# Optimization experiments

Measured on AMD Instinct MI355X. Metric: run time of the kernel, lower is better.

The kernel has to match this reference:

```python
import jax, jax.numpy as jnp
import numpy as np

H = 4096          # hidden_size
I = 11008         # intermediate_size
G = 128           # AWQ group_size
# AWQ interleaved nibble order within each packed int32
_ORDER = jnp.array([0, 4, 1, 5, 2, 6, 3, 7], dtype=jnp.int32) * 4


def _mk_lin(key, K, N):
    k1, k2, k3 = jax.random.split(key, 3)
    qw = jax.random.randint(k1, (K, N // 8), 0, 100, dtype=jnp.int32)
    qz = jax.random.randint(k2, (K // G, N // 8), 0, 100, dtype=jnp.int32)
    sc = jax.random.normal(k3, (K // G, N), dtype=jnp.float32) * 0.02
    return qw, qz, sc


def setup_inputs() -> dict:
    key = jax.random.key(0)
    ks = jax.random.split(key, 7)
    x = jax.random.normal(ks[0], (8, 16, H), dtype=jnp.float32)
    ln1_w = jnp.ones((H,), dtype=jnp.float32)
    ln2_w = jnp.ones((H,), dtype=jnp.float32)
    qkv_qw, qkv_qz, qkv_sc = _mk_lin(ks[1], H, 3 * H)
    o_qw, o_qz, o_sc = _mk_lin(ks[2], H, H)
    gu_qw, gu_qz, gu_sc = _mk_lin(ks[3], H, 2 * I)
    dn_qw, dn_qz, dn_sc = _mk_lin(ks[4], I, H)
    return dict(x=x, ln1_w=ln1_w, ln2_w=ln2_w,
                qkv_qw=qkv_qw, qkv_qz=qkv_qz, qkv_sc=qkv_sc,
                o_qw=o_qw, o_qz=o_qz, o_sc=o_sc,
                gu_qw=gu_qw, gu_qz=gu_qz, gu_sc=gu_sc,
                dn_qw=dn_qw, dn_qz=dn_qz, dn_sc=dn_sc)


def rmsnorm(x, w, eps=1e-6):
    return x * jax.lax.rsqrt(jnp.mean(x * x, axis=-1, keepdims=True) + eps) * w


def dequant(qw, qz, sc):
    # qw: [K, N//8] int32 -> [K, N]; qz: [K//G, N//8] -> [K//G, N]
    K = qw.shape[0]
    N = sc.shape[1]
    w = ((qw[:, :, None] >> _ORDER) & 0xF).reshape(K, N).astype(sc.dtype)
    z = ((qz[:, :, None] >> _ORDER) & 0xF).reshape(K // G, N).astype(sc.dtype)
    return (w - jnp.repeat(z, G, axis=0)) * jnp.repeat(sc, G, axis=0)


def lite_linear(x, qw, qz, sc):
    return x @ dequant(qw, qz, sc)


def reference(x, ln1_w, ln2_w,
              qkv_qw, qkv_qz, qkv_sc,
              o_qw, o_qz, o_sc,
              gu_qw, gu_qz, gu_sc,
              dn_qw, dn_qz, dn_sc):
    residual = x
    h = rmsnorm(x, ln1_w)
    h = lite_linear(h, qkv_qw, qkv_qz, qkv_sc)[..., :H]  # mock attn: take q slice
    h = lite_linear(h, o_qw, o_qz, o_sc)
    h = residual + h
    residual = h
    h = rmsnorm(h, ln2_w)
    gate_up = lite_linear(h, gu_qw, gu_qz, gu_sc)
    gate, up = gate_up[..., :I], gate_up[..., I:]
    h = lite_linear(jax.nn.silu(gate) * up, dn_qw, dn_qz, dn_sc)
    return residual + h
```

## Files before the change

kernel.cpp:

```cpp
#include <hip/hip_runtime.h>

typedef unsigned int   u32;
typedef unsigned short u16;

typedef _Float16 h2  __attribute__((ext_vector_type(2)));
typedef _Float16 h8  __attribute__((ext_vector_type(8)));
typedef float    f32x4 __attribute__((ext_vector_type(4)));

#define M_TOK 128

__device__ __forceinline__ u16 f2h_(float f) {
    _Float16 h = (_Float16)f; return __builtin_bit_cast(u16, h);
}
__device__ __forceinline__ float h2f_(u16 b) {
    _Float16 h = __builtin_bit_cast(_Float16, b); return (float)h;
}
__device__ __forceinline__ void acc8(uint4 v, float* s) {
#pragma unroll
    for (int i = 0; i < 4; ++i) {
        u32 w = ((const u32*)&v)[i];
        s[2 * i]     += h2f_((u16)(w & 0xFFFF));
        s[2 * i + 1] += h2f_((u16)(w >> 16));
    }
}

__constant__ int SHC[8] = {0, 16, 4, 20, 8, 24, 12, 28};

__launch_bounds__(256)
__global__ void pack_zs(const int* __restrict__ qz, const float* __restrict__ sc,
                        u32* __restrict__ zs, int qws, int scs, int Ncols, int total) {
    const int idx = blockIdx.x * 256 + threadIdx.x;
    if (idx >= total) return;
    const int g = idx / Ncols, n = idx - g * Ncols;
    const u32 d = (u32)qz[(size_t)g * qws + (n >> 3)];
    const u32 zj = (d >> SHC[n & 7]) & 15u;
    const u32 mz = 0xE400u | zj;
    const u16 sh = f2h_(sc[(size_t)g * scs + n]);
    zs[(size_t)g * Ncols + n] = mz | ((u32)sh << 16);
}


__launch_bounds__(256)
__global__ void rmsnorm_k(const float* __restrict__ in, const float* __restrict__ w,
                          u16* __restrict__ out) {
    const int row = blockIdx.x;
    const float* x = in + (size_t)row * 4096;
    float ss = 0.f;
#pragma unroll
    for (int j = 0; j < 16; ++j) {
        float v = x[threadIdx.x + 256 * j];
        ss += v * v;
    }
#pragma unroll
    for (int off = 32; off > 0; off >>= 1) ss += __shfl_down(ss, off, 64);
    __shared__ float ws4[4];
    if ((threadIdx.x & 63) == 0) ws4[threadIdx.x >> 6] = ss;
    __syncthreads();
    float total = ws4[0] + ws4[1] + ws4[2] + ws4[3];
    float r = rsqrtf(total * (1.f / 4096.f) + 1e-6f);
    const int mt = row >> 4, l16 = row & 15;
#pragma unroll
    for (int c2 = 0; c2 < 2; ++c2) {
        int c = threadIdx.x * 2 + c2;
        int kb = c >> 2, qq = c & 3;
        u16 o8[8];
#pragma unroll
        for (int j = 0; j < 8; ++j) {
            int i = c * 8 + j;
            o8[j] = f2h_(x[i] * r * w[i]);
        }
        *(uint4*)(out + ((size_t)(kb * 8 + mt) * 64 + qq * 16 + l16) * 8) = *(const uint4*)o8;
    }
}

__launch_bounds__(256, 2)
__global__ void gemm_awq(const u16* __restrict__ A, const u32* __restrict__ zs,
                         const int* __restrict__ qw, u16* __restrict__ part,
                         int qws, int N, int K, int kchunk) {
    __shared__ __align__(16) char ldsB[4 * 4608];

    const int tid = threadIdx.x, w = tid >> 6, lane = tid & 63;
    const int q = lane >> 4, l16 = lane & 15;
    const int n0w = blockIdx.x * 128 + w * 32;
    const int pc0 = n0w >> 3;
    const int kp = lane & 31, h = lane >> 5;
    const int sk = blockIdx.y, kc0 = sk * kchunk, kend = min(kc0 + kchunk, K);

    char* myB   = ldsB + w * 4608;
    char* wbase = myB + kp * 4;
    const u16* Ala = A + lane * 8;
    const int* qws_base = qw + pc0;
    const u32* zsA = zs + n0w + h * 8;
    const u32* zsB = zs + n0w + 16 + h * 8;

    f32x4 acc[8][2] = {};
    uint4 za0, za1, zb0, zb1;

    auto ldraw = [&](int k0) -> uint4 {
        return *(const uint4*)(qws_base + (size_t)(k0 + lane) * qws);
    };
    auto loadzs = [&](int g) {
        za0 = *(const uint4*)(zsA + (size_t)g * N);
        za1 = *(const uint4*)(zsA + (size_t)g * N + 4);
        zb0 = *(const uint4*)(zsB + (size_t)g * N);
        zb1 = *(const uint4*)(zsB + (size_t)g * N + 4);
    };
    auto route = [&](uint4 rv, u32* d) {
        const int i0 = kp * 8, i1 = i0 + 4;
        int b00 = __builtin_amdgcn_ds_bpermute(i0, (int)rv.x);
        int b10 = __builtin_amdgcn_ds_bpermute(i0, (int)rv.y);
        int b20 = __builtin_amdgcn_ds_bpermute(i0, (int)rv.z);
        int b30 = __builtin_amdgcn_ds_bpermute(i0, (int)rv.w);
        int b01 = __builtin_amdgcn_ds_bpermute(i1, (int)rv.x);
        int b11 = __builtin_amdgcn_ds_bpermute(i1, (int)rv.y);
        int b21 = __builtin_amdgcn_ds_bpermute(i1, (int)rv.z);
        int b31 = __builtin_amdgcn_ds_bpermute(i1, (int)rv.w);
        d[0] = (u32)(h ? b10 : b00);
        d[1] = (u32)(h ? b11 : b01);
        d[2] = (u32)(h ? b30 : b20);
        d[3] = (u32)(h ? b31 : b21);
    };
    auto emit8 = [&](u32 w0, u32 w1, int nb, uint4 z0, uint4 z1) {
        char* bb = wbase + nb * 144;
        u32 w0s = w0 >> 4, w1s = w1 >> 4;
        auto em = [&](int j, u32 a0, u32 a1, int b, u32 zsj) {
            h2 mz = __builtin_bit_cast(h2, __builtin_amdgcn_perm(zsj, zsj, 0x01000100u));
            h2 s2 = __builtin_bit_cast(h2, __builtin_amdgcn_perm(zsj, zsj, 0x03020302u));
            u32 t = __builtin_amdgcn_perm(a1, a0, (u32)(b | ((b + 4) << 16)));
            u32 u = (t & 0x000F000Fu) | 0x64006400u;
            h2 v = (__builtin_bit_cast(h2, u) + mz) * s2;
            *(u32*)(bb + j * 144) = __builtin_bit_cast(u32, v);
        };
        em(0, w0, w1, 0, z0.x);  em(4, w0, w1, 1, z1.x);
        em(1, w0, w1, 2, z0.y);  em(5, w0, w1, 3, z1.y);
        em(2, w0s, w1s, 0, z0.z); em(6, w0s, w1s, 1, z1.z);
        em(3, w0s, w1s, 2, z0.w); em(7, w0s, w1s, 3, z1.w);
    };
    auto lda = [&](int k, uint4(&dst)[2][8]) {
        const int kb = k >> 5;
#pragma unroll
        for (int c = 0; c < 2; ++c)
#pragma unroll
            for (int mt = 0; mt < 8; ++mt)
                dst[c][mt] = *(const uint4*)(Ala + (size_t)((kb + c) * 8 + mt) * 512);
    };

    uint4 afA[2][8], afB[2][8];
    uint4 rv_n = {0,0,0,0};

    loadzs(kc0 >> 7);
    uint4 rv0 = ldraw(kc0);
    if (kc0 + 64 < kend) rv_n = ldraw(kc0 + 64);
    lda(kc0, afA);
    {
        u32 qd[4];
        route(rv0, qd);
        emit8(qd[0], qd[1], h * 8, za0, za1);
        emit8(qd[2], qd[3], 16 + h * 8, zb0, zb1);
    }
    if (((kc0 + 64) & 127) == 0 && kc0 + 64 < kend)
        loadzs((kc0 + 64) >> 7);

    auto step = [&](int k0, uint4(&cur)[2][8], uint4(&nxt)[2][8]) {
        const bool kn1 = (k0 + 64) < kend, kn2 = (k0 + 128) < kend;
        if (kn1) lda(k0 + 64, nxt);
        uint4 bv[2][2];
#pragma unroll
        for (int c = 0; c < 2; ++c)
#pragma unroll
            for (int nt = 0; nt < 2; ++nt)
                bv[c][nt] = *(const uint4*)(myB + (nt * 16 + l16) * 144 + c * 64 + q * 16);
        uint4 rv_f = {0,0,0,0};
        if (kn2) rv_f = ldraw(k0 + 128);
        if (kn1) {
            u32 qd[4];
            route(rv_n, qd);
            emit8(qd[0], qd[1], h * 8, za0, za1);
            emit8(qd[2], qd[3], 16 + h * 8, zb0, zb1);
        }
        if (kn2 && (((k0 + 128) & 127) == 0))
            loadzs((k0 + 128) >> 7);
#pragma unroll
        for (int c = 0; c < 2; ++c)
#pragma unroll
            for (int mt = 0; mt < 8; ++mt)
#pragma unroll
                for (int nt = 0; nt < 2; ++nt)
                    acc[mt][nt] = __builtin_amdgcn_mfma_f32_16x16x32_f16(
                        __builtin_bit_cast(h8, cur[c][mt]),
                        __builtin_bit_cast(h8, bv[c][nt]),
                        acc[mt][nt], 0, 0, 0);
        rv_n = rv_f;
    };
    for (int k0 = kc0; k0 < kend; k0 += 128) {
        step(k0, afA, afB);
        if (k0 + 64 < kend) step(k0 + 64, afB, afA);
    }

    u16* pp = part + (size_t)sk * M_TOK * N;
#pragma unroll
    for (int mt = 0; mt < 8; ++mt)
#pragma unroll
        for (int nt = 0; nt < 2; ++nt) {
            const int n = n0w + nt * 16 + l16;
#pragma unroll
            for (int r = 0; r < 4; ++r) {
                const int m = mt * 16 + q * 4 + r;
                pp[(size_t)m * N + n] = f2h_(acc[mt][nt][r]);
            }
        }
}

__launch_bounds__(256)
__global__ void reduce_to_afrag(const u16* __restrict__ part, u16* __restrict__ out,
                                int SK) {
    const int idx = blockIdx.x * 256 + threadIdx.x;
    const int m = idx >> 9, c = idx & 511;
    float s[8] = {};
    for (int k = 0; k < SK; ++k)
        acc8(*(const uint4*)(part + (size_t)k * 524288 + (size_t)m * 4096 + c * 8), s);
    const int kb = c >> 2, qq = c & 3, mt = m >> 4, l16 = m & 15;
    u16 o8[8];
#pragma unroll
    for (int j = 0; j < 8; ++j) o8[j] = f2h_(s[j]);
    *(uint4*)(out + ((size_t)(kb * 8 + mt) * 64 + qq * 16 + l16) * 8) = *(const uint4*)o8;
}

__launch_bounds__(256)
__global__ void reduce_add_f32(const u16* __restrict__ part, const float* __restrict__ resin,
                               float* __restrict__ out, int SK) {
    const int idx = blockIdx.x * 256 + threadIdx.x;
    const size_t base = (size_t)idx * 8;
    float s[8];
    *(float4*)&s[0] = *(const float4*)(resin + base);
    *(float4*)&s[4] = *(const float4*)(resin + base + 4);
    for (int k = 0; k < SK; ++k)
        acc8(*(const uint4*)(part + (size_t)k * 524288 + base), s);
    *(float4*)(out + base)     = *(const float4*)&s[0];
    *(float4*)(out + base + 4) = *(const float4*)&s[4];
}

__launch_bounds__(256)
__global__ void silu_mul(const u16* __restrict__ part, u16* __restrict__ act) {
    const int idx = blockIdx.x * 256 + threadIdx.x;
    const int m = idx / 1376, c = idx - m * 1376;
    const int nb = c * 8;
    float g[8] = {}, u[8] = {};
    for (int k = 0; k < 3; ++k) {
        const size_t base = (size_t)k * 2818048 + (size_t)m * 22016 + nb;
        acc8(*(const uint4*)(part + base), g);
        acc8(*(const uint4*)(part + base + 11008), u);
    }
    const int kb = nb >> 5, qq = (nb >> 3) & 3, mt = m >> 4, l16 = m & 15;
    u16 o8[8];
#pragma unroll
    for (int j = 0; j < 8; ++j) {
        float a = g[j] / (1.f + __expf(-g[j])) * u[j];
        o8[j] = f2h_(a);
    }
    *(uint4*)(act + ((size_t)(kb * 8 + mt) * 64 + qq * 16 + l16) * 8) = *(const uint4*)o8;
}

extern "C" void kernel_launch(void* const* d_in, const int* in_sizes, int n_in,
                              void* d_out, int out_size, void* d_ws, size_t ws_size,
                              hipStream_t stream) {
    const float* x      = (const float*)d_in[0];
    const float* ln1_w  = (const float*)d_in[1];
    const float* ln2_w  = (const float*)d_in[2];
    const int*   qkv_qw = (const int*)d_in[3];
    const int*   qkv_qz = (const int*)d_in[4];
    const float* qkv_sc = (const float*)d_in[5];
    const int*   o_qw   = (const int*)d_in[6];
    const int*   o_qz   = (const int*)d_in[7];
    const float* o_sc   = (const float*)d_in[8];
    const int*   gu_qw  = (const int*)d_in[9];
    const int*   gu_qz  = (const int*)d_in[10];
    const float* gu_sc  = (const float*)d_in[11];
    const int*   dn_qw  = (const int*)d_in[12];
    const int*   dn_qz  = (const int*)d_in[13];
    const float* dn_sc  = (const float*)d_in[14];
    float* out = (float*)d_out;

    char* ws = (char*)d_ws;
    u16*   pbuf = (u16*)(ws);
    u32*   zsb  = (u32*)(ws + 16908288);
    u16*   act  = (u16*)(ws + 19726336);
    float* res2 = (float*)(ws + 22544384);
    u16*   slot = (u16*)(ws + 24641536);

    rmsnorm_k<<<128, 256, 0, stream>>>(x, ln1_w, slot);
    pack_zs<<<512, 256, 0, stream>>>(qkv_qz, qkv_sc, zsb, 1536, 12288, 4096, 131072);

    gemm_awq<<<dim3(32, 16), 256, 0, stream>>>(slot, zsb, qkv_qw, pbuf,
                                               1536, 4096, 4096, 256);
    reduce_to_afrag<<<256, 256, 0, stream>>>(pbuf, slot, 16);
    pack_zs<<<512, 256, 0, stream>>>(o_qz, o_sc, zsb, 512, 4096, 4096, 131072);

    gemm_awq<<<dim3(32, 16), 256, 0, stream>>>(slot, zsb, o_qw, pbuf,
                                               512, 4096, 4096, 256);
    reduce_add_f32<<<256, 256, 0, stream>>>(pbuf, x, res2, 16);

    rmsnorm_k<<<128, 256, 0, stream>>>(res2, ln2_w, slot);
    pack_zs<<<2752, 256, 0, stream>>>(gu_qz, gu_sc, zsb, 2752, 22016, 22016, 704512);

    gemm_awq<<<dim3(172, 3), 256, 0, stream>>>(slot, zsb, gu_qw, pbuf,
                                               2752, 22016, 4096, 1408);
    silu_mul<<<688, 256, 0, stream>>>(pbuf, act);
    pack_zs<<<1376, 256, 0, stream>>>(dn_qz, dn_sc, zsb, 512, 4096, 4096, 352256);

    gemm_awq<<<dim3(32, 16), 256, 0, stream>>>(act, zsb, dn_qw, pbuf,
                                               512, 4096, 11008, 704);
    reduce_add_f32<<<256, 256, 0, stream>>>(pbuf, res2, out, 16);
}
```

Before: 303.7 us.

## Repack AWQ weights into lane-ordered layout to drop in-kernel bpermute routing

Adds a repack_qw kernel that rearranges each layer's packed int4 weights into a per-lane uint4 layout before its GEMM. A templated gemm_awq<1> then reads one contiguous uint4 per lane and skips the eight ds_bpermute shuffles used to route nibbles. This removes cross-lane shuffle and LDS traffic from the GEMM inner loop. In exchange, every call pays an extra full read and write of the weights into workspace. The repacked path is only taken when the workspace is large enough.

```diff
diff --git a/kernel.cpp b/kernel.cpp
--- a/kernel.cpp
+++ b/kernel.cpp
@@ -39,6 +39,24 @@
     zs[(size_t)g * Ncols + n] = mz | ((u32)sh << 16);
 }
 
+__launch_bounds__(256)
+__global__ void repack_qw(const int* __restrict__ qw, uint4* __restrict__ qout,
+                          int qws, int ST ) {
+    const int t = threadIdx.x;
+    const int j = t >> 6, lane = t & 63;
+    const int kp = lane & 31, h = lane >> 5;
+    const int g = blockIdx.x * 4 + j;
+    const int s = blockIdx.y;
+    const int r0 = s * 64 + kp * 2;
+    const int* base = qw + (size_t)r0 * qws + 4 * g + h;
+    uint4 o;
+    o.x = (u32)base[0];
+    o.y = (u32)base[qws];
+    o.z = (u32)base[2];
+    o.w = (u32)base[qws + 2];
+    qout[((size_t)g * ST + s) * 64 + lane] = o;
+}
+
 
 __launch_bounds__(256)
 __global__ void rmsnorm_k(const float* __restrict__ in, const float* __restrict__ w,
@@ -73,9 +91,10 @@
     }
 }
 
+template<int RP>
 __launch_bounds__(256, 2)
 __global__ void gemm_awq(const u16* __restrict__ A, const u32* __restrict__ zs,
-                         const int* __restrict__ qw, u16* __restrict__ part,
+                         const void* __restrict__ qwv, u16* __restrict__ part,
                          int qws, int N, int K, int kchunk) {
     __shared__ __align__(16) char ldsB[4 * 4608];
 
@@ -89,7 +108,8 @@
     char* myB   = ldsB + w * 4608;
     char* wbase = myB + kp * 4;
     const u16* Ala = A + lane * 8;
-    const int* qws_base = qw + pc0;
+    const int* qws_base = (const int*)qwv + pc0;
+    const uint4* qrp = (const uint4*)qwv + (size_t)(n0w >> 5) * (K >> 6) * 64 + lane;
     const u32* zsA = zs + n0w + h * 8;
     const u32* zsB = zs + n0w + 16 + h * 8;
 
@@ -97,6 +117,7 @@
     uint4 za0, za1, zb0, zb1;
 
     auto ldraw = [&](int k0) -> uint4 {
+        if (RP) return qrp[(size_t)(k0 >> 6) * 64];
         return *(const uint4*)(qws_base + (size_t)(k0 + lane) * qws);
     };
     auto loadzs = [&](int g) {
@@ -136,6 +157,13 @@
         em(2, w0s, w1s, 0, z0.z); em(6, w0s, w1s, 1, z1.z);
         em(3, w0s, w1s, 2, z0.w); em(7, w0s, w1s, 3, z1.w);
     };
+    auto dq = [&](uint4 rv) {
+        u32 qd[4];
+        if (RP) { qd[0] = rv.x; qd[1] = rv.y; qd[2] = rv.z; qd[3] = rv.w; }
+        else route(rv, qd);
+        emit8(qd[0], qd[1], h * 8, za0, za1);
+        emit8(qd[2], qd[3], 16 + h * 8, zb0, zb1);
+    };
     auto lda = [&](int k, uint4(&dst)[2][8]) {
         const int kb = k >> 5;
 #pragma unroll
@@ -146,18 +174,13 @@
     };
 
     uint4 afA[2][8], afB[2][8];
-    uint4 rv_n = {0,0,0,0};
+    uint4 rv_n = {0, 0, 0, 0};
 
     loadzs(kc0 >> 7);
     uint4 rv0 = ldraw(kc0);
     if (kc0 + 64 < kend) rv_n = ldraw(kc0 + 64);
     lda(kc0, afA);
-    {
-        u32 qd[4];
-        route(rv0, qd);
-        emit8(qd[0], qd[1], h * 8, za0, za1);
-        emit8(qd[2], qd[3], 16 + h * 8, zb0, zb1);
-    }
+    dq(rv0);
     if (((kc0 + 64) & 127) == 0 && kc0 + 64 < kend)
         loadzs((kc0 + 64) >> 7);
 
@@ -170,14 +193,9 @@
 #pragma unroll
             for (int nt = 0; nt < 2; ++nt)
                 bv[c][nt] = *(const uint4*)(myB + (nt * 16 + l16) * 144 + c * 64 + q * 16);
-        uint4 rv_f = {0,0,0,0};
+        uint4 rv_f = {0, 0, 0, 0};
         if (kn2) rv_f = ldraw(k0 + 128);
-        if (kn1) {
-            u32 qd[4];
-            route(rv_n, qd);
-            emit8(qd[0], qd[1], h * 8, za0, za1);
-            emit8(qd[2], qd[3], 16 + h * 8, zb0, zb1);
-        }
+        if (kn1) dq(rv_n);
         if (kn2 && (((k0 + 128) & 127) == 0))
             loadzs((k0 + 128) >> 7);
 #pragma unroll
@@ -287,28 +305,55 @@
     u16*   act  = (u16*)(ws + 19726336);
     float* res2 = (float*)(ws + 22544384);
     u16*   slot = (u16*)(ws + 24641536);
+    uint4* qwr  = (uint4*)(ws + 25690112);
+    const bool rp_full = ws_size >= 70778880u;
+    const bool rp_mid  = ws_size >= 48234496u;
 
     rmsnorm_k<<<128, 256, 0, stream>>>(x, ln1_w, slot);
     pack_zs<<<512, 256, 0, stream>>>(qkv_qz, qkv_sc, zsb, 1536, 12288, 4096, 131072);
 
-    gemm_awq<<<dim3(32, 16), 256, 0, stream>>>(slot, zsb, qkv_qw, pbuf,
-                                               1536, 4096, 4096, 256);
+    if (rp_mid) {
+        repack_qw<<<dim3(32, 64), 256, 0, stream>>>(qkv_qw, qwr, 1536, 64);
+        gemm_awq<1><<<dim3(32, 16), 256, 0, stream>>>(slot, zsb, qwr, pbuf,
+                                                      1536, 4096, 4096, 256);
+    } else {
+        gemm_awq<0><<<dim3(32, 16), 256, 0, stream>>>(slot, zsb, qkv_qw, pbuf,
+                                                      1536, 4096, 4096, 256);
+    }
     reduce_to_afrag<<<256, 256, 0, stream>>>(pbuf, slot, 16);
     pack_zs<<<512, 256, 0, stream>>>(o_qz, o_sc, zsb, 512, 4096, 4096, 131072);
 
-    gemm_awq<<<dim3(32, 16), 256, 0, stream>>>(slot, zsb, o_qw, pbuf,
-                                               512, 4096, 4096, 256);
+    if (rp_mid) {
+        repack_qw<<<dim3(32, 64), 256, 0, stream>>>(o_qw, qwr, 512, 64);
+        gemm_awq<1><<<dim3(32, 16), 256, 0, stream>>>(slot, zsb, qwr, pbuf,
+                                                      512, 4096, 4096, 256);
+    } else {
+        gemm_awq<0><<<dim3(32, 16), 256, 0, stream>>>(slot, zsb, o_qw, pbuf,
+                                                      512, 4096, 4096, 256);
+    }
     reduce_add_f32<<<256, 256, 0, stream>>>(pbuf, x, res2, 16);
 
     rmsnorm_k<<<128, 256, 0, stream>>>(res2, ln2_w, slot);
     pack_zs<<<2752, 256, 0, stream>>>(gu_qz, gu_sc, zsb, 2752, 22016, 22016, 704512);
 
-    gemm_awq<<<dim3(172, 3), 256, 0, stream>>>(slot, zsb, gu_qw, pbuf,
-                                               2752, 22016, 4096, 1408);
+    if (rp_full) {
+        repack_qw<<<dim3(172, 64), 256, 0, stream>>>(gu_qw, qwr, 2752, 64);
+        gemm_awq<1><<<dim3(172, 3), 256, 0, stream>>>(slot, zsb, qwr, pbuf,
+                                                      2752, 22016, 4096, 1408);
+    } else {
+        gemm_awq<0><<<dim3(172, 3), 256, 0, stream>>>(slot, zsb, gu_qw, pbuf,
+                                                      2752, 22016, 4096, 1408);
+    }
     silu_mul<<<688, 256, 0, stream>>>(pbuf, act);
     pack_zs<<<1376, 256, 0, stream>>>(dn_qz, dn_sc, zsb, 512, 4096, 4096, 352256);
 
-    gemm_awq<<<dim3(32, 16), 256, 0, stream>>>(act, zsb, dn_qw, pbuf,
-                                               512, 4096, 11008, 704);
+    if (rp_mid) {
+        repack_qw<<<dim3(32, 172), 256, 0, stream>>>(dn_qw, qwr, 512, 172);
+        gemm_awq<1><<<dim3(32, 16), 256, 0, stream>>>(act, zsb, qwr, pbuf,
+                                                      512, 4096, 11008, 704);
+    } else {
+        gemm_awq<0><<<dim3(32, 16), 256, 0, stream>>>(act, zsb, dn_qw, pbuf,
+                                                      512, 4096, 11008, 704);
+    }
     reduce_add_f32<<<256, 256, 0, stream>>>(pbuf, res2, out, 16);
 }
```

Measured after the change: 339.2 us. 1.12x slower.
